# Performance work log

Hardware: AMD Instinct MI355X
Metric: run time of the kernel (lower is better)

## Reference

```python
import jax, jax.numpy as jnp
import numpy as np

EPS = 1e-6
NUM_HEADS = 8
NUM_TOKENS = 196

def setup_inputs() -> dict:
    key = jax.random.key(0)
    ks = jax.random.split(key, 4)
    B, N, C = 32, 3136, 384
    H, Dh, M = NUM_HEADS, C // NUM_HEADS, NUM_TOKENS
    return {
        "x": jax.random.normal(ks[0], (B, N, C), dtype=jnp.float32),
        "q_param": jax.random.normal(ks[1], (1, M, H, Dh), dtype=jnp.float32) * 0.02,
        "kv_w": jax.random.normal(ks[2], (2 * C, C), dtype=jnp.float32) * 0.02,
        "proj_w": jax.random.normal(ks[3], (C, C), dtype=jnp.float32) * 0.02,
        "proj_b": jnp.zeros((C,), dtype=jnp.float32),
        "ln_w": jnp.ones((C,), dtype=jnp.float32),
        "ln_b": jnp.zeros((C,), dtype=jnp.float32),
    }

def reference(x, q_param, kv_w, proj_w, proj_b, ln_w, ln_b):
    B, N, C = x.shape
    H = NUM_HEADS
    Dh = C // H
    # LayerNorm (eps=1e-6)
    mu = jnp.mean(x, axis=-1, keepdims=True)
    var = jnp.mean(jnp.square(x - mu), axis=-1, keepdims=True)
    x = (x - mu) * jax.lax.rsqrt(var + EPS) * ln_w + ln_b
    # exact GELU (nn.GELU default)
    x = jax.nn.gelu(x, approximate=False)
    # kv projection (no bias): [B,N,2C] -> k,v each [B,H,N,Dh]
    kv = (x @ kv_w.T).reshape(B, N, 2, H, Dh)
    kv = jnp.transpose(kv, (2, 0, 3, 1, 4))
    k, v = kv[0], kv[1]
    # learnable queries: (1,M,H,Dh) -> (1,H,M,Dh)
    q = jnp.transpose(q_param, (0, 2, 1, 3))
    # NOTE: source applies NO 1/sqrt(Dh) scaling
    attn = jnp.einsum("bhmd,bhnd->bhmn", jnp.broadcast_to(q, (B, H, NUM_TOKENS, Dh)), k)
    attn = jax.nn.softmax(attn, axis=-1)
    out = jnp.einsum("bhmn,bhnd->bhmd", attn, v)  # [B,H,M,Dh]
    out = jnp.transpose(out, (0, 2, 1, 3)).reshape(B, NUM_TOKENS, C)
    return out @ proj_w.T + proj_b
```

## Files before the change

### kernel.cpp

```cpp
#include <hip/hip_runtime.h>
#include <stdint.h>

typedef float f32x4 __attribute__((ext_vector_type(4)));
typedef short s16x8 __attribute__((ext_vector_type(8)));
typedef short s16x4 __attribute__((ext_vector_type(4)));
typedef unsigned short ushort_t;

#define B_  32
#define N_  3136
#define C_  384
#define H_  8
#define DH_ 48
#define M_  196
#define ROWS  (B_*N_)
#define PROWS (B_*M_)
#define NCHUNK 4

static __device__ __forceinline__ ushort_t f2bf(float f) {
  union { float f; uint32_t u; } v; v.f = f;
  uint32_t r = (v.u + 0x7fffu + ((v.u >> 16) & 1u)) >> 16;
  return (ushort_t)r;
}
static __device__ __forceinline__ ushort_t f2bf_fast(float f) {
  union { float f; uint32_t u; } v; v.f = f;
  return (ushort_t)((v.u + 0x8000u) >> 16);
}

static __device__ __forceinline__ f32x4 mfma_16x16x32(s16x8 a, s16x8 b, f32x4 c) {
  return __builtin_amdgcn_mfma_f32_16x16x32_bf16(a, b, c, 0, 0, 0);
}

static __device__ __forceinline__ f32x4 mfma_16x16x16(s16x4 a, s16x4 b, f32x4 c) {
#if __has_builtin(__builtin_amdgcn_mfma_f32_16x16x16_bf16)
  return __builtin_amdgcn_mfma_f32_16x16x16_bf16(a, b, c, 0, 0, 0);
#elif __has_builtin(__builtin_amdgcn_mfma_f32_16x16x16bf16_1k)
  return __builtin_amdgcn_mfma_f32_16x16x16bf16_1k(a, b, c, 0, 0, 0);
#else
  f32x4 d;
  asm("v_mfma_f32_16x16x16_bf16 %0, %1, %2, %3" : "=v"(d) : "v"(a), "v"(b), "v"(c));
  return d;
#endif
}

static __device__ __forceinline__ void gload_lds16(const void* g, void* l) {
  __builtin_amdgcn_global_load_lds(
      (const __attribute__((address_space(1))) void*)(uintptr_t)g,
      (__attribute__((address_space(3))) void*)(uint32_t)(uintptr_t)l,
      16, 0, 0);
}

__global__ __launch_bounds__(256) void k_ln_gelu(
    const float* __restrict__ x, const float* __restrict__ lnw,
    const float* __restrict__ lnb, ushort_t* __restrict__ x16) {
  int row = blockIdx.x * 4 + (threadIdx.x >> 6);
  int lane = threadIdx.x & 63;
  const float2* xr = (const float2*)(x + (size_t)row * C_);
  float2 v0 = xr[lane], v1 = xr[lane + 64], v2 = xr[lane + 128];
  float s  = v0.x + v0.y + v1.x + v1.y + v2.x + v2.y;
  float ss = v0.x*v0.x + v0.y*v0.y + v1.x*v1.x + v1.y*v1.y + v2.x*v2.x + v2.y*v2.y;
#pragma unroll
  for (int off = 1; off < 64; off <<= 1) {
    s  += __shfl_xor(s, off);
    ss += __shfl_xor(ss, off);
  }
  float mu = s * (1.0f / C_);
  float rs = rsqrtf(ss * (1.0f / C_) - mu * mu + 1e-6f);
  const float2* wr = (const float2*)lnw;
  const float2* br = (const float2*)lnb;
  uint32_t* outp = (uint32_t*)(x16 + (size_t)row * C_);
#pragma unroll
  for (int t = 0; t < 3; ++t) {
    int idx = lane + t * 64;
    float2 v = (t == 0) ? v0 : ((t == 1) ? v1 : v2);
    float2 w = wr[idx], bb = br[idx];
    float a0 = (v.x - mu) * rs * w.x + bb.x;
    float a1 = (v.y - mu) * rs * w.y + bb.y;
    a0 = 0.5f * a0 * (1.0f + erff(a0 * 0.70710678118654752440f));
    a1 = 0.5f * a1 * (1.0f + erff(a1 * 0.70710678118654752440f));
    outp[idx] = (uint32_t)f2bf_fast(a0) | ((uint32_t)f2bf_fast(a1) << 16);
  }
}

__global__ __launch_bounds__(256) void k_convert(
    const float* __restrict__ kvw, const float* __restrict__ pw,
    const float* __restrict__ qp, ushort_t* __restrict__ wkv16,
    ushort_t* __restrict__ wp16, ushort_t* __restrict__ q16) {
  int i = blockIdx.x * 256 + threadIdx.x;
  if (i < 2 * C_ * C_) wkv16[i] = f2bf(kvw[i]);
  if (i < C_ * C_)     wp16[i]  = f2bf(pw[i]);
  if (i < M_ * H_ * DH_) {
    int d = i % DH_; int t = i / DH_; int h = t % H_; int m = t / H_;
    q16[((size_t)h * M_ + m) * DH_ + d] = f2bf(qp[i]);
  }
}

template <typename OutT, bool BIAS, bool SWZ>
__global__ __launch_bounds__(256) void k_gemm_bt(
    const ushort_t* __restrict__ A, const ushort_t* __restrict__ Bw,
    OutT* __restrict__ Co, const float* __restrict__ bias,
    int M, int N, int K, int ntn) {
  __shared__ ushort_t lA[2][128 * 32];
  __shared__ ushort_t lB[2][128 * 32];
  int bid = blockIdx.x;
  if (SWZ) bid = (bid & 7) * (gridDim.x >> 3) + (bid >> 3);
  int tr = bid / ntn, tc = bid % ntn;
  int tid = threadIdx.x;
  int w = tid >> 6, l = tid & 63;
  int wr = w >> 1, wc = w & 1;
  int c = l & 15, g = l >> 4;
  f32x4 acc[4][4];
#pragma unroll
  for (int i = 0; i < 4; ++i)
#pragma unroll
    for (int j = 0; j < 4; ++j) acc[i][j] = (f32x4){0.f, 0.f, 0.f, 0.f};
  const size_t a0 = (size_t)tr * 128, b0 = (size_t)tc * 128;
  int srow = l >> 2;
  int scol = (l & 3) * 8;
#pragma unroll
  for (int r = 0; r < 2; ++r) {
    int lr = w * 16 + r * 64;
    gload_lds16(A  + (a0 + lr + srow) * (size_t)K + scol, &lA[0][lr * 32]);
    gload_lds16(Bw + (b0 + lr + srow) * (size_t)K + scol, &lB[0][lr * 32]);
  }
  const int T = K >> 5;
  for (int t = 0; t < T; ++t) {
    int cur = t & 1;
    if (t + 1 < T) {
      int kt = (t + 1) << 5;
#pragma unroll
      for (int r = 0; r < 2; ++r) {
        int lr = w * 16 + r * 64;
        gload_lds16(A  + (a0 + lr + srow) * (size_t)K + kt + scol, &lA[cur ^ 1][lr * 32]);
        gload_lds16(Bw + (b0 + lr + srow) * (size_t)K + kt + scol, &lB[cur ^ 1][lr * 32]);
      }
      asm volatile("s_waitcnt vmcnt(4)" ::: "memory");
    } else {
      asm volatile("s_waitcnt vmcnt(0)" ::: "memory");
    }
    __builtin_amdgcn_sched_barrier(0);
    __builtin_amdgcn_s_barrier();
    s16x8 af[4], bf[4];
#pragma unroll
    for (int i = 0; i < 4; ++i)
      af[i] = *(const s16x8*)&lA[cur][(wr * 64 + i * 16 + c) * 32 + g * 8];
#pragma unroll
    for (int j = 0; j < 4; ++j)
      bf[j] = *(const s16x8*)&lB[cur][(wc * 64 + j * 16 + c) * 32 + g * 8];
#pragma unroll
    for (int i = 0; i < 4; ++i)
#pragma unroll
      for (int j = 0; j < 4; ++j)
        acc[i][j] = mfma_16x16x32(af[i], bf[j], acc[i][j]);
    __builtin_amdgcn_sched_barrier(0);
    __builtin_amdgcn_s_barrier();
  }
#pragma unroll
  for (int i = 0; i < 4; ++i) {
#pragma unroll
    for (int j = 0; j < 4; ++j) {
      size_t col = b0 + wc * 64 + j * 16 + c;
      float bs = BIAS ? bias[col] : 0.0f;
#pragma unroll
      for (int q = 0; q < 4; ++q) {
        size_t row = a0 + wr * 64 + i * 16 + g * 4 + q;
        float v = acc[i][j][q] + bs;
        if constexpr (sizeof(OutT) == 2) Co[row * N + col] = f2bf(v);
        else                             Co[row * N + col] = v;
      }
    }
  }
}

__global__ __launch_bounds__(512) void k_attn(
    const ushort_t* __restrict__ kv, const ushort_t* __restrict__ q16,
    float* __restrict__ Opart, float2* __restrict__ mlp) {
  int slot = blockIdx.x;
  int chunk = slot & (NCHUNK - 1), bh = slot >> 2;
  int b = bh >> 3, h = bh & 7;
  int tile0 = (chunk == 0) ? 0 : (12 * chunk + 1);
  int tile1 = tile0 + ((chunk == 0) ? 13 : 12);
  __shared__ ushort_t Kl[64 * 72];
  __shared__ ushort_t Vt[48 * 76];
  int tid = threadIdx.x;
  int w = tid >> 6, l = tid & 63;
  int c = l & 15, g = l >> 4;
  for (int i = tid; i < 64 * 72; i += 512) Kl[i] = 0;
  for (int i = tid; i < 48 * 76; i += 512) Vt[i] = 0;
  s16x8 qf[2][2];
#pragma unroll
  for (int i = 0; i < 2; ++i)
#pragma unroll
    for (int kk = 0; kk < 2; ++kk) {
      int m = w * 32 + i * 16 + c;
      int dh = kk * 32 + g * 8;
      s16x8 z = {0, 0, 0, 0, 0, 0, 0, 0};
      qf[i][kk] = (m < M_ && dh < DH_)
                      ? *(const s16x8*)(q16 + ((size_t)h * M_ + m) * DH_ + dh)
                      : z;
    }
  f32x4 o[3][2];
#pragma unroll
  for (int f = 0; f < 3; ++f)
#pragma unroll
    for (int i = 0; i < 2; ++i) o[f][i] = (f32x4){0.f, 0.f, 0.f, 0.f};
  float rm[2] = {-3e38f, -3e38f}, rl[2] = {0.f, 0.f};
  int srow = tid >> 3, spart = tid & 7;
  const size_t rowstride = (size_t)(2 * C_);
  uint32_t kr0, kr1, kr2, vr0, vr1, vr2;
  {
    size_t gb = ((size_t)b * N_ + tile0 * 64 + srow) * rowstride + h * DH_ + spart * 6;
    kr0 = *(const uint32_t*)(kv + gb);
    kr1 = *(const uint32_t*)(kv + gb + 2);
    kr2 = *(const uint32_t*)(kv + gb + 4);
    vr0 = *(const uint32_t*)(kv + gb + C_);
    vr1 = *(const uint32_t*)(kv + gb + C_ + 2);
    vr2 = *(const uint32_t*)(kv + gb + C_ + 4);
  }
  __syncthreads();

  for (int t = tile0; t < tile1; ++t) {
    uint32_t* kd = (uint32_t*)&Kl[srow * 72 + spart * 6];
    kd[0] = kr0; kd[1] = kr1; kd[2] = kr2;
    int dbase = spart * 6;
    Vt[(dbase + 0) * 76 + srow] = (ushort_t)vr0;
    Vt[(dbase + 1) * 76 + srow] = (ushort_t)(vr0 >> 16);
    Vt[(dbase + 2) * 76 + srow] = (ushort_t)vr1;
    Vt[(dbase + 3) * 76 + srow] = (ushort_t)(vr1 >> 16);
    Vt[(dbase + 4) * 76 + srow] = (ushort_t)vr2;
    Vt[(dbase + 5) * 76 + srow] = (ushort_t)(vr2 >> 16);
    __syncthreads();
    {
      int tn = (t < tile1 - 1) ? t + 1 : t;
      size_t gb = ((size_t)b * N_ + tn * 64 + srow) * rowstride + h * DH_ + spart * 6;
      kr0 = *(const uint32_t*)(kv + gb);
      kr1 = *(const uint32_t*)(kv + gb + 2);
      kr2 = *(const uint32_t*)(kv + gb + 4);
      vr0 = *(const uint32_t*)(kv + gb + C_);
      vr1 = *(const uint32_t*)(kv + gb + C_ + 2);
      vr2 = *(const uint32_t*)(kv + gb + C_ + 4);
    }
    f32x4 s[4][2];
#pragma unroll
    for (int j = 0; j < 4; ++j) {
      s16x8 kf0 = *(const s16x8*)&Kl[(j * 16 + c) * 72 + g * 8];
      s16x8 kf1 = *(const s16x8*)&Kl[(j * 16 + c) * 72 + 32 + g * 8];
#pragma unroll
      for (int i = 0; i < 2; ++i) {
        f32x4 z = {0.f, 0.f, 0.f, 0.f};
        f32x4 t0 = mfma_16x16x32(kf0, qf[i][0], z);
        s[j][i] = mfma_16x16x32(kf1, qf[i][1], t0);
      }
    }
    s16x4 pb[2][4];
#pragma unroll
    for (int i = 0; i < 2; ++i) {
      float tm = s[0][i][0];
#pragma unroll
      for (int j = 0; j < 4; ++j)
#pragma unroll
        for (int q = 0; q < 4; ++q) tm = fmaxf(tm, s[j][i][q]);
      tm = fmaxf(tm, __shfl_xor(tm, 16));
      tm = fmaxf(tm, __shfl_xor(tm, 32));
      float nm = fmaxf(rm[i], tm);
      float corr = __expf(rm[i] - nm);
      rm[i] = nm;
      float ts = 0.f;
#pragma unroll
      for (int j = 0; j < 4; ++j) {
        float p0 = __expf(s[j][i][0] - nm);
        float p1 = __expf(s[j][i][1] - nm);
        float p2 = __expf(s[j][i][2] - nm);
        float p3 = __expf(s[j][i][3] - nm);
        ts += (p0 + p1) + (p2 + p3);
        pb[i][j] = (s16x4){(short)f2bf_fast(p0), (short)f2bf_fast(p1),
                           (short)f2bf_fast(p2), (short)f2bf_fast(p3)};
      }
      ts += __shfl_xor(ts, 16);
      ts += __shfl_xor(ts, 32);
      rl[i] = rl[i] * corr + ts;
#pragma unroll
      for (int f = 0; f < 3; ++f) o[f][i] *= corr;
    }
#pragma unroll
    for (int f = 0; f < 3; ++f)
#pragma unroll
      for (int j = 0; j < 4; ++j) {
        s16x4 vf = *(const s16x4*)&Vt[(f * 16 + c) * 76 + j * 16 + g * 4];
        o[f][0] = mfma_16x16x16(vf, pb[0][j], o[f][0]);
        o[f][1] = mfma_16x16x16(vf, pb[1][j], o[f][1]);
      }
    __syncthreads();
  }
#pragma unroll
  for (int i = 0; i < 2; ++i) {
    int m = w * 32 + i * 16 + c;
    if (m < M_) {
#pragma unroll
      for (int f = 0; f < 3; ++f)
        *(f32x4*)&Opart[((size_t)slot * M_ + m) * 48 + f * 16 + g * 4] = o[f][i];
      if (g == 0) {
        float2 v; v.x = rm[i]; v.y = rl[i];
        mlp[slot * M_ + m] = v;
      }
    }
  }
}

__global__ __launch_bounds__(256) void k_combine(
    const float* __restrict__ Opart, const float2* __restrict__ mlp,
    ushort_t* __restrict__ att16) {
  int wid = blockIdx.x * 4 + (threadIdx.x >> 6);
  int lane = threadIdx.x & 63;
  int bh = wid / M_, m = wid - bh * M_;
  int b = bh >> 3, h = bh & 7;
  float mc[NCHUNK], lc[NCHUNK];
#pragma unroll
  for (int cc = 0; cc < NCHUNK; ++cc) {
    float2 v = mlp[(bh * NCHUNK + cc) * M_ + m];
    mc[cc] = v.x; lc[cc] = v.y;
  }
  float Mx = fmaxf(fmaxf(mc[0], mc[1]), fmaxf(mc[2], mc[3]));
  float L = 0.f, sc[NCHUNK];
#pragma unroll
  for (int cc = 0; cc < NCHUNK; ++cc) {
    sc[cc] = __expf(mc[cc] - Mx);
    L += sc[cc] * lc[cc];
  }
  if (lane < 48) {
    float od = 0.f;
#pragma unroll
    for (int cc = 0; cc < NCHUNK; ++cc)
      od += sc[cc] * Opart[((size_t)(bh * NCHUNK + cc) * M_ + m) * 48 + lane];
    att16[((size_t)b * M_ + m) * C_ + h * DH_ + lane] = f2bf_fast(od / L);
  }
}

extern "C" void kernel_launch(void* const* d_in, const int* in_sizes, int n_in,
                              void* d_out, int out_size, void* d_ws, size_t ws_size,
                              hipStream_t stream) {
  (void)in_sizes; (void)n_in; (void)out_size; (void)ws_size;
  const float* x   = (const float*)d_in[0];
  const float* qp  = (const float*)d_in[1];
  const float* kvw = (const float*)d_in[2];
  const float* pw  = (const float*)d_in[3];
  const float* pbv = (const float*)d_in[4];
  const float* lnw = (const float*)d_in[5];
  const float* lnb = (const float*)d_in[6];
  float* out = (float*)d_out;

  ushort_t* x16   = (ushort_t*)d_ws;
  ushort_t* kv16  = x16 + (size_t)ROWS * C_;
  ushort_t* att16 = kv16 + (size_t)ROWS * 2 * C_;
  ushort_t* wkv16 = att16 + (size_t)PROWS * C_;
  ushort_t* wp16  = wkv16 + 2 * C_ * C_;
  ushort_t* q16   = wp16 + C_ * C_;
  float*  Opart = (float*)d_ws;
  float2* mlp   = (float2*)(Opart + (size_t)(B_ * H_ * NCHUNK) * M_ * 48);

  hipLaunchKernelGGL(k_ln_gelu, dim3(ROWS / 4), dim3(256), 0, stream, x, lnw, lnb, x16);
  hipLaunchKernelGGL(k_convert, dim3((2 * C_ * C_ + 255) / 256), dim3(256), 0, stream,
                     kvw, pw, qp, wkv16, wp16, q16);
  hipLaunchKernelGGL((k_gemm_bt<ushort_t, false, true>),
                     dim3((ROWS / 128) * (2 * C_ / 128)), dim3(256), 0, stream,
                     x16, wkv16, kv16, (const float*)nullptr, ROWS, 2 * C_, C_, 2 * C_ / 128);
  hipLaunchKernelGGL(k_attn, dim3(B_ * H_ * NCHUNK), dim3(512), 0, stream,
                     kv16, q16, Opart, mlp);
  hipLaunchKernelGGL(k_combine, dim3(B_ * H_ * M_ / 4), dim3(256), 0, stream,
                     Opart, mlp, att16);
  hipLaunchKernelGGL((k_gemm_bt<float, true, false>),
                     dim3((PROWS / 128) * (C_ / 128)), dim3(256), 0, stream,
                     att16, wp16, out, pbv, PROWS, C_, C_, C_ / 128);
}
```

Before: 272.0 us.

## Triple-buffer GEMM LDS tiles and XOR-swizzle rows to avoid bank conflicts

The bf16 GEMM's LDS staging goes from two buffers to three, so global-to-LDS loads for the tile two iterations ahead can be in flight while the current tile is computed. The waitcnt thresholds are adjusted to match the deeper prefetch. The 16-byte column chunks within each row are also XOR-swizzled by row bits, on both the direct-to-LDS load side and the fragment read side, to reduce LDS bank conflicts. This costs more shared memory per block, which may lower occupancy.

```diff
diff --git a/kernel.cpp b/kernel.cpp
--- a/kernel.cpp
+++ b/kernel.cpp
@@ -99,8 +99,8 @@
     const ushort_t* __restrict__ A, const ushort_t* __restrict__ Bw,
     OutT* __restrict__ Co, const float* __restrict__ bias,
     int M, int N, int K, int ntn) {
-  __shared__ ushort_t lA[2][128 * 32];
-  __shared__ ushort_t lB[2][128 * 32];
+  __shared__ ushort_t lA[3][128 * 32];
+  __shared__ ushort_t lB[3][128 * 32];
   int bid = blockIdx.x;
   if (SWZ) bid = (bid & 7) * (gridDim.x >> 3) + (bid >> 3);
   int tr = bid / ntn, tc = bid % ntn;
@@ -115,24 +115,35 @@
     for (int j = 0; j < 4; ++j) acc[i][j] = (f32x4){0.f, 0.f, 0.f, 0.f};
   const size_t a0 = (size_t)tr * 128, b0 = (size_t)tc * 128;
   int srow = l >> 2;
-  int scol = (l & 3) * 8;
+  int scol = (((l & 3) ^ ((l >> 3) & 3))) * 8;
+  const int rsw = (c >> 1) & 3;
+  const int T = K >> 5;
 #pragma unroll
   for (int r = 0; r < 2; ++r) {
     int lr = w * 16 + r * 64;
     gload_lds16(A  + (a0 + lr + srow) * (size_t)K + scol, &lA[0][lr * 32]);
     gload_lds16(Bw + (b0 + lr + srow) * (size_t)K + scol, &lB[0][lr * 32]);
   }
-  const int T = K >> 5;
+  if (T > 1) {
+#pragma unroll
+    for (int r = 0; r < 2; ++r) {
+      int lr = w * 16 + r * 64;
+      gload_lds16(A  + (a0 + lr + srow) * (size_t)K + 32 + scol, &lA[1][lr * 32]);
+      gload_lds16(Bw + (b0 + lr + srow) * (size_t)K + 32 + scol, &lB[1][lr * 32]);
+    }
+  }
+  int cur = 0, nxt2 = 2;
   for (int t = 0; t < T; ++t) {
-    int cur = t & 1;
-    if (t + 1 < T) {
-      int kt = (t + 1) << 5;
+    if (t + 2 < T) {
+      int kt = (t + 2) << 5;
 #pragma unroll
       for (int r = 0; r < 2; ++r) {
         int lr = w * 16 + r * 64;
-        gload_lds16(A  + (a0 + lr + srow) * (size_t)K + kt + scol, &lA[cur ^ 1][lr * 32]);
-        gload_lds16(Bw + (b0 + lr + srow) * (size_t)K + kt + scol, &lB[cur ^ 1][lr * 32]);
-      }
+        gload_lds16(A  + (a0 + lr + srow) * (size_t)K + kt + scol, &lA[nxt2][lr * 32]);
+        gload_lds16(Bw + (b0 + lr + srow) * (size_t)K + kt + scol, &lB[nxt2][lr * 32]);
+      }
+      asm volatile("s_waitcnt vmcnt(8)" ::: "memory");
+    } else if (t + 1 < T) {
       asm volatile("s_waitcnt vmcnt(4)" ::: "memory");
     } else {
       asm volatile("s_waitcnt vmcnt(0)" ::: "memory");
@@ -141,11 +152,15 @@
     __builtin_amdgcn_s_barrier();
     s16x8 af[4], bf[4];
 #pragma unroll
-    for (int i = 0; i < 4; ++i)
-      af[i] = *(const s16x8*)&lA[cur][(wr * 64 + i * 16 + c) * 32 + g * 8];
-#pragma unroll
-    for (int j = 0; j < 4; ++j)
-      bf[j] = *(const s16x8*)&lB[cur][(wc * 64 + j * 16 + c) * 32 + g * 8];
+    for (int i = 0; i < 4; ++i) {
+      int row = wr * 64 + i * 16 + c;
+      af[i] = *(const s16x8*)&lA[cur][row * 32 + ((unsigned)(g ^ rsw)) * 8];
+    }
+#pragma unroll
+    for (int j = 0; j < 4; ++j) {
+      int row = wc * 64 + j * 16 + c;
+      bf[j] = *(const s16x8*)&lB[cur][row * 32 + ((unsigned)(g ^ rsw)) * 8];
+    }
 #pragma unroll
     for (int i = 0; i < 4; ++i)
 #pragma unroll
@@ -153,6 +168,8 @@
         acc[i][j] = mfma_16x16x32(af[i], bf[j], acc[i][j]);
     __builtin_amdgcn_sched_barrier(0);
     __builtin_amdgcn_s_barrier();
+    cur = (cur == 2) ? 0 : cur + 1;
+    nxt2 = (nxt2 == 2) ? 0 : nxt2 + 1;
   }
 #pragma unroll
   for (int i = 0; i < 4; ++i) {
```

After: 266.4 us. 2.1% less time.
